# Performance work log

Measured on AMD Instinct MI355X. Metric: run time of the kernel, lower is better.

The kernel has to match this reference:

```python
import jax, jax.numpy as jnp
import numpy as np

N_NODES = 100000
N_EDGES = 1600000
IN_DIM = 128
HID_DIM = 64
OUT_DIM = 1


def setup_inputs() -> dict:
    key = jax.random.key(0)
    k = jax.random.split(key, 8)
    x = jax.random.normal(k[0], (N_NODES, IN_DIM), dtype=jnp.float32)
    edge_index = jax.random.randint(k[1], (2, N_EDGES), 0, N_NODES, dtype=jnp.int64)
    # GCNConv layer 1: weight [IN, HID], bias [HID] (glorot-ish scale)
    W1 = jax.random.normal(k[2], (IN_DIM, HID_DIM), dtype=jnp.float32) / np.sqrt(IN_DIM)
    b1 = jnp.zeros((HID_DIM,), dtype=jnp.float32)
    W2 = jax.random.normal(k[3], (HID_DIM, HID_DIM), dtype=jnp.float32) / np.sqrt(HID_DIM)
    b2 = jnp.zeros((HID_DIM,), dtype=jnp.float32)
    Wfc = jax.random.normal(k[4], (HID_DIM, OUT_DIM), dtype=jnp.float32) / np.sqrt(HID_DIM)
    bfc = jnp.zeros((OUT_DIM,), dtype=jnp.float32)
    return {"x": x, "edge_index": edge_index, "W1": W1, "b1": b1,
            "W2": W2, "b2": b2, "Wfc": Wfc, "bfc": bfc}


def _gcn_norm(edge_index, n_nodes):
    # PyG GCNConv default: add self-loops, symmetric normalization.
    src, dst = edge_index[0], edge_index[1]
    loop = jnp.arange(n_nodes, dtype=src.dtype)
    src = jnp.concatenate([src, loop])
    dst = jnp.concatenate([dst, loop])
    deg = jax.ops.segment_sum(jnp.ones_like(dst, dtype=jnp.float32), dst,
                              num_segments=n_nodes)
    deg_isqrt = jax.lax.rsqrt(deg)  # deg >= 1 thanks to self-loops
    norm = deg_isqrt[src] * deg_isqrt[dst]  # [E+N]
    return src, dst, norm


def _gcn_conv(x, src, dst, norm, W, b, n_nodes):
    h = x @ W                      # [N, D_out] dense transform first (D_out <= D_in)
    msg = h[src] * norm[:, None]   # gather + normalize  [E+N, D_out]
    out = jax.ops.segment_sum(msg, dst, num_segments=n_nodes)  # scatter-add
    return out + b


def reference(x, edge_index, W1, b1, W2, b2, Wfc, bfc):
    n = x.shape[0]
    src, dst, norm = _gcn_norm(edge_index, n)
    h = jax.nn.relu(_gcn_conv(x, src, dst, norm, W1, b1, n))
    h = jax.nn.relu(_gcn_conv(h, src, dst, norm, W2, b2, n))
    return h @ Wfc + bfc  # [N, 1]
```

## Files before the change

### kernel.cpp

```cpp
#include <hip/hip_runtime.h>
#include <hip/hip_bf16.h>


#define IN_DIM 128
#define HID 64
#define B1 256
#define MAXNC 128

typedef unsigned int uint;

__device__ inline uint pack_bf16x2(float a, float b) {
    uint ua = __builtin_bit_cast(uint, a);
    uint ub = __builtin_bit_cast(uint, b);
    ua += 0x7fffu + ((ua >> 16) & 1u);
    ub += 0x7fffu + ((ub >> 16) & 1u);
    return (ua >> 16) | (ub & 0xffff0000u);
}
__device__ inline float bf_lo(uint g) { return __builtin_bit_cast(float, g << 16); }
__device__ inline float bf_hi(uint g) { return __builtin_bit_cast(float, g & 0xffff0000u); }

__global__ __launch_bounds__(512) void hist1(const int* __restrict__ dst,
                                             int* __restrict__ ghist,
                                             int E, int NC, int chunk) {
    __shared__ int h[MAXNC];
    int t = threadIdx.x, blk = blockIdx.x;
    if (t < NC) h[t] = 0;
    __syncthreads();
    int s = blk * chunk, e = min(E, s + chunk);
    for (int i = s + t; i < e; i += 512) atomicAdd(&h[dst[i] >> 10], 1);
    __syncthreads();
    if (t < NC) ghist[(size_t)t * B1 + blk] = h[t];
}

__global__ __launch_bounds__(1024) void scan_mat(int* __restrict__ a, int M,
                                                 int* __restrict__ row_off, int N) {
    __shared__ int ws[16], wsoff[16], total_s;
    int t = threadIdx.x;
    int seg = (M + 1023) >> 10;
    int s = t * seg, e = min(M, s + seg);
    int sum = 0;
    for (int i = s; i < e; ++i) sum += a[i];
    int incl = sum;
#pragma unroll
    for (int o = 1; o < 64; o <<= 1) {
        int u = __shfl_up(incl, o, 64);
        if ((t & 63) >= o) incl += u;
    }
    if ((t & 63) == 63) ws[t >> 6] = incl;
    __syncthreads();
    if (t == 0) {
        int run = 0;
#pragma unroll
        for (int i = 0; i < 16; ++i) { wsoff[i] = run; run += ws[i]; }
        total_s = run;
    }
    __syncthreads();
    int run = wsoff[t >> 6] + incl - sum;
    for (int i = s; i < e; ++i) { int tmp = a[i]; a[i] = run; run += tmp; }
    if (t == 0) row_off[N] = total_s;
}

__global__ __launch_bounds__(512) void scatter1(const int* __restrict__ src,
                                                const int* __restrict__ dst,
                                                const int* __restrict__ goff,
                                                int2* __restrict__ pairs,
                                                int E, int NC, int chunk) {
    __shared__ int cur[MAXNC];
    int t = threadIdx.x, blk = blockIdx.x;
    if (t < NC) cur[t] = goff[(size_t)t * B1 + blk];
    __syncthreads();
    int s = blk * chunk, e = min(E, s + chunk);
    for (int i = s + t; i < e; i += 512) {
        int d = dst[i];
        int p = atomicAdd(&cur[d >> 10], 1);
        pairs[p] = make_int2(src[i], d);
    }
}

__global__ __launch_bounds__(1024) void build_csr(const int2* __restrict__ pairs,
                                                  const int* __restrict__ goff,
                                                  int* __restrict__ row_off,
                                                  float* __restrict__ disqrt,
                                                  int* __restrict__ col,
                                                  int E, int NC, int N) {
    __shared__ int h[1024], cur[1024];
    __shared__ int ws[16], wsoff[16];
    int b = blockIdx.x, t = threadIdx.x;
    int base = goff[(size_t)b * B1];
    int next = (b + 1 < NC) ? goff[(size_t)(b + 1) * B1] : E;
    h[t] = 0;
    __syncthreads();
    for (int i = base + t; i < next; i += 1024)
        atomicAdd(&h[pairs[i].y & 1023], 1);
    __syncthreads();
    int deg = h[t];
    int incl = deg;
#pragma unroll
    for (int o = 1; o < 64; o <<= 1) {
        int u = __shfl_up(incl, o, 64);
        if ((t & 63) >= o) incl += u;
    }
    if ((t & 63) == 63) ws[t >> 6] = incl;
    __syncthreads();
    if (t == 0) {
        int run = 0;
#pragma unroll
        for (int i = 0; i < 16; ++i) { wsoff[i] = run; run += ws[i]; }
    }
    __syncthreads();
    int excl = wsoff[t >> 6] + incl - deg;
    cur[t] = base + excl;
    int node = (b << 10) + t;
    if (node < N) {
        row_off[node] = base + excl;
        disqrt[node]  = rsqrtf((float)(deg + 1));
    }
    __syncthreads();
    for (int i = base + t; i < next; i += 1024) {
        int2 p = pairs[i];
        int pos = atomicAdd(&cur[p.y & 1023], 1);
        col[pos] = p.x;
    }
}

template <int K>
__global__ __launch_bounds__(256) void gemm_tile(const float* __restrict__ X,
                                                 const float* __restrict__ W,
                                                 const float* __restrict__ disqrt,
                                                 uint* __restrict__ Tsb, int n) {
    __shared__ float xs[32][68];
    __shared__ float ws[32][64];
    const int tid  = threadIdx.x;
    const int nIdx = tid & 15;
    const int mIdx = tid >> 4;
    const int m0   = blockIdx.x * 64;
    float acc[4][4] = {};
    for (int kc = 0; kc < K; kc += 32) {
        int f = tid;
#pragma unroll
        for (int i = 0; i < 2; ++i, f += 256) {
            int r  = f >> 3;
            int kq = f & 7;
            int row = m0 + r;
            float4 g = make_float4(0.f, 0.f, 0.f, 0.f);
            if (row < n) g = *(const float4*)(X + (size_t)row * K + kc + 4 * kq);
            xs[4 * kq + 0][r] = g.x;
            xs[4 * kq + 1][r] = g.y;
            xs[4 * kq + 2][r] = g.z;
            xs[4 * kq + 3][r] = g.w;
        }
        f = tid;
#pragma unroll
        for (int i = 0; i < 2; ++i, f += 256) {
            int kk = f >> 4;
            int cq = f & 15;
            *(float4*)&ws[kk][4 * cq] =
                *(const float4*)(W + (size_t)(kc + kk) * 64 + 4 * cq);
        }
        __syncthreads();
#pragma unroll 4
        for (int k = 0; k < 32; ++k) {
            float4 a = *(const float4*)&xs[k][4 * mIdx];
            float4 b = *(const float4*)&ws[k][4 * nIdx];
            const float* ap = (const float*)&a;
            const float* bp = (const float*)&b;
#pragma unroll
            for (int mi = 0; mi < 4; ++mi)
#pragma unroll
                for (int ni = 0; ni < 4; ++ni)
                    acc[mi][ni] += ap[mi] * bp[ni];
        }
        __syncthreads();
    }
#pragma unroll
    for (int mi = 0; mi < 4; ++mi) {
        int row = m0 + 4 * mIdx + mi;
        if (row < n) {
            float s = disqrt[row];
            uint2 pk;
            pk.x = pack_bf16x2(acc[mi][0] * s, acc[mi][1] * s);
            pk.y = pack_bf16x2(acc[mi][2] * s, acc[mi][3] * s);
            *(uint2*)(Tsb + (size_t)row * 32 + 2 * nIdx) = pk;
        }
    }
}

template <bool FUSE_FC>
__global__ __launch_bounds__(256) void agg_kernel(const uint* __restrict__ Tsb,
                                                  const int* __restrict__ row_off,
                                                  const int* __restrict__ col,
                                                  const float* __restrict__ disqrt,
                                                  const float* __restrict__ bias,
                                                  const float* __restrict__ wfc,
                                                  const float* __restrict__ bfc,
                                                  float* __restrict__ out, int n) {
    int node = blockIdx.x * 4 + (threadIdx.x >> 6);
    if (node >= n) return;
    int lane = threadIdx.x & 63;
    int h = lane >> 5;
    int p = lane & 31;
    float2 acc = make_float2(0.f, 0.f);
    {
        uint g = Tsb[(size_t)node * 32 + p];
        if (h == 0) { acc.x += bf_lo(g); acc.y += bf_hi(g); }
    }
    int beg = __builtin_amdgcn_readfirstlane(row_off[node]);
    int end = __builtin_amdgcn_readfirstlane(row_off[node + 1]);
    int i = beg;
    for (; i + 8 <= end; i += 8) {
        int e = i + h;
        int s0 = col[e + 0];
        int s1 = col[e + 2];
        int s2 = col[e + 4];
        int s3 = col[e + 6];
        uint g0 = Tsb[(size_t)s0 * 32 + p];
        uint g1 = Tsb[(size_t)s1 * 32 + p];
        uint g2 = Tsb[(size_t)s2 * 32 + p];
        uint g3 = Tsb[(size_t)s3 * 32 + p];
        acc.x += bf_lo(g0); acc.y += bf_hi(g0);
        acc.x += bf_lo(g1); acc.y += bf_hi(g1);
        acc.x += bf_lo(g2); acc.y += bf_hi(g2);
        acc.x += bf_lo(g3); acc.y += bf_hi(g3);
    }
    for (; i + 2 <= end; i += 2) {
        int s = col[i + h];
        uint g = Tsb[(size_t)s * 32 + p];
        acc.x += bf_lo(g); acc.y += bf_hi(g);
    }
    if (i < end) {
        int s = col[i];
        uint g = Tsb[(size_t)s * 32 + p];
        if (h == 0) { acc.x += bf_lo(g); acc.y += bf_hi(g); }
    }
    acc.x += __shfl_xor(acc.x, 32, 64);
    acc.y += __shfl_xor(acc.y, 32, 64);
    float dq = disqrt[node];
    float2 bv = *(const float2*)(bias + 2 * p);
    float rx = fmaxf(acc.x * dq + bv.x, 0.f);
    float ry = fmaxf(acc.y * dq + bv.y, 0.f);
    if (!FUSE_FC) {
        if (h == 0)
            *(float2*)(out + (size_t)node * HID + 2 * p) = make_float2(rx, ry);
    } else {
        float2 wv = *(const float2*)(wfc + 2 * p);
        float v = rx * wv.x + ry * wv.y;
        v += __shfl_down(v, 16, 64);
        v += __shfl_down(v, 8, 64);
        v += __shfl_down(v, 4, 64);
        v += __shfl_down(v, 2, 64);
        v += __shfl_down(v, 1, 64);
        if (lane == 0) out[node] = v + bfc[0];
    }
}

extern "C" void kernel_launch(void* const* d_in, const int* in_sizes, int n_in,
                              void* d_out, int out_size, void* d_ws, size_t ws_size,
                              hipStream_t stream) {
    const float* x   = (const float*)d_in[0];
    const int*   ei  = (const int*)d_in[1];
    const float* W1  = (const float*)d_in[2];
    const float* b1  = (const float*)d_in[3];
    const float* W2  = (const float*)d_in[4];
    const float* b2  = (const float*)d_in[5];
    const float* Wfc = (const float*)d_in[6];
    const float* bfc = (const float*)d_in[7];
    float* out = (float*)d_out;

    const int N = in_sizes[0] / IN_DIM;
    const int E = in_sizes[1] / 2;
    const int* src = ei;
    const int* dst = ei + E;
    const int NC    = (N + 1023) >> 10;
    const int chunk = (E + B1 - 1) / B1;

    char* w = (char*)d_ws;
    auto alloc = [&](size_t bytes) {
        void* p = (void*)w;
        w += (bytes + 255) & ~(size_t)255;
        return p;
    };
    int*   row_off = (int*)alloc((size_t)(N + 1) * 4);
    float* disqrt  = (float*)alloc((size_t)N * 4);
    int*   goff    = (int*)alloc((size_t)NC * B1 * 4);
    int*   col     = (int*)alloc((size_t)E * 4);
    size_t scrA = (size_t)E * 8, scrB = (size_t)N * HID * 2;
    void*  scr  = alloc(scrA > scrB ? scrA : scrB);
    float* h1   = (float*)alloc((size_t)N * HID * 4);
    int2*  pairs = (int2*)scr;
    uint*  Tsb   = (uint*)scr;

    hist1<<<B1, 512, 0, stream>>>(dst, goff, E, NC, chunk);
    scan_mat<<<1, 1024, 0, stream>>>(goff, NC * B1, row_off, N);
    scatter1<<<B1, 512, 0, stream>>>(src, dst, goff, pairs, E, NC, chunk);
    build_csr<<<NC, 1024, 0, stream>>>(pairs, goff, row_off, disqrt, col, E, NC, N);

    gemm_tile<IN_DIM><<<(N + 63) / 64, 256, 0, stream>>>(x, W1, disqrt, Tsb, N);
    agg_kernel<false><<<(N + 3) / 4, 256, 0, stream>>>(Tsb, row_off, col, disqrt,
                                                       b1, nullptr, nullptr, h1, N);

    gemm_tile<HID><<<(N + 63) / 64, 256, 0, stream>>>(h1, W2, disqrt, Tsb, N);
    agg_kernel<true><<<(N + 3) / 4, 256, 0, stream>>>(Tsb, row_off, col, disqrt,
                                                      b2, Wfc, bfc, out, N);
}
```

Measured before the change: 320.1 us.

## Prefetch GEMM tiles into registers and batch column-index loads via wave shuffles

The GEMM kernel now loads the next K-chunk of X and W into registers while the current shared-memory tile is being consumed, which overlaps global loads with FMAs. The inner loop unroll also rises to 8. The aggregation kernel loads up to 64 column indices per wave with one coalesced load and hands them out with shuffles, and it unrolls to 8 outstanding gathers per half-wave, which cuts dependent index-load latency. The cost is higher register pressure and extra shuffle instructions.

```diff
diff --git a/kernel.cpp b/kernel.cpp
--- a/kernel.cpp
+++ b/kernel.cpp
@@ -134,31 +134,34 @@
     const int nIdx = tid & 15;
     const int mIdx = tid >> 4;
     const int m0   = blockIdx.x * 64;
+    const int r0 = tid >> 3, kq = tid & 7, r1 = r0 + 32;
+    const int wk = tid >> 4, wc = tid & 15;
+    const int row0 = m0 + r0, row1 = m0 + r1;
+    const float4 z4 = make_float4(0.f, 0.f, 0.f, 0.f);
+
+    float4 gx0 = (row0 < n) ? *(const float4*)(X + (size_t)row0 * K + 4 * kq) : z4;
+    float4 gx1 = (row1 < n) ? *(const float4*)(X + (size_t)row1 * K + 4 * kq) : z4;
+    float4 gw0 = *(const float4*)(W + (size_t)wk * 64 + 4 * wc);
+    float4 gw1 = *(const float4*)(W + (size_t)(wk + 16) * 64 + 4 * wc);
+
     float acc[4][4] = {};
-    for (int kc = 0; kc < K; kc += 32) {
-        int f = tid;
-#pragma unroll
-        for (int i = 0; i < 2; ++i, f += 256) {
-            int r  = f >> 3;
-            int kq = f & 7;
-            int row = m0 + r;
-            float4 g = make_float4(0.f, 0.f, 0.f, 0.f);
-            if (row < n) g = *(const float4*)(X + (size_t)row * K + kc + 4 * kq);
-            xs[4 * kq + 0][r] = g.x;
-            xs[4 * kq + 1][r] = g.y;
-            xs[4 * kq + 2][r] = g.z;
-            xs[4 * kq + 3][r] = g.w;
-        }
-        f = tid;
-#pragma unroll
-        for (int i = 0; i < 2; ++i, f += 256) {
-            int kk = f >> 4;
-            int cq = f & 15;
-            *(float4*)&ws[kk][4 * cq] =
-                *(const float4*)(W + (size_t)(kc + kk) * 64 + 4 * cq);
-        }
+    for (int kc = 0;;) {
+        xs[4 * kq + 0][r0] = gx0.x; xs[4 * kq + 1][r0] = gx0.y;
+        xs[4 * kq + 2][r0] = gx0.z; xs[4 * kq + 3][r0] = gx0.w;
+        xs[4 * kq + 0][r1] = gx1.x; xs[4 * kq + 1][r1] = gx1.y;
+        xs[4 * kq + 2][r1] = gx1.z; xs[4 * kq + 3][r1] = gx1.w;
+        *(float4*)&ws[wk][4 * wc]      = gw0;
+        *(float4*)&ws[wk + 16][4 * wc] = gw1;
         __syncthreads();
-#pragma unroll 4
+        kc += 32;
+        const bool more = kc < K;
+        if (more) {
+            gx0 = (row0 < n) ? *(const float4*)(X + (size_t)row0 * K + kc + 4 * kq) : z4;
+            gx1 = (row1 < n) ? *(const float4*)(X + (size_t)row1 * K + kc + 4 * kq) : z4;
+            gw0 = *(const float4*)(W + (size_t)(kc + wk) * 64 + 4 * wc);
+            gw1 = *(const float4*)(W + (size_t)(kc + wk + 16) * 64 + 4 * wc);
+        }
+#pragma unroll 8
         for (int k = 0; k < 32; ++k) {
             float4 a = *(const float4*)&xs[k][4 * mIdx];
             float4 b = *(const float4*)&ws[k][4 * nIdx];
@@ -170,6 +173,7 @@
                 for (int ni = 0; ni < 4; ++ni)
                     acc[mi][ni] += ap[mi] * bp[ni];
         }
+        if (!more) break;
         __syncthreads();
     }
 #pragma unroll
@@ -202,35 +206,51 @@
     float2 acc = make_float2(0.f, 0.f);
     {
         uint g = Tsb[(size_t)node * 32 + p];
-        if (h == 0) { acc.x += bf_lo(g); acc.y += bf_hi(g); }
+        if (h == 0) { acc.x = bf_lo(g); acc.y = bf_hi(g); }
     }
     int beg = __builtin_amdgcn_readfirstlane(row_off[node]);
     int end = __builtin_amdgcn_readfirstlane(row_off[node + 1]);
-    int i = beg;
-    for (; i + 8 <= end; i += 8) {
-        int e = i + h;
-        int s0 = col[e + 0];
-        int s1 = col[e + 2];
-        int s2 = col[e + 4];
-        int s3 = col[e + 6];
-        uint g0 = Tsb[(size_t)s0 * 32 + p];
-        uint g1 = Tsb[(size_t)s1 * 32 + p];
-        uint g2 = Tsb[(size_t)s2 * 32 + p];
-        uint g3 = Tsb[(size_t)s3 * 32 + p];
-        acc.x += bf_lo(g0); acc.y += bf_hi(g0);
-        acc.x += bf_lo(g1); acc.y += bf_hi(g1);
-        acc.x += bf_lo(g2); acc.y += bf_hi(g2);
-        acc.x += bf_lo(g3); acc.y += bf_hi(g3);
-    }
-    for (; i + 2 <= end; i += 2) {
-        int s = col[i + h];
-        uint g = Tsb[(size_t)s * 32 + p];
-        acc.x += bf_lo(g); acc.y += bf_hi(g);
-    }
-    if (i < end) {
-        int s = col[i];
-        uint g = Tsb[(size_t)s * 32 + p];
-        if (h == 0) { acc.x += bf_lo(g); acc.y += bf_hi(g); }
+    for (int batch = beg; batch < end; batch += 64) {
+        int bn = min(64, end - batch);
+        int cv = 0;
+        if (batch + lane < end) cv = col[batch + lane];
+        int j = 0;
+        for (; j + 16 <= bn; j += 16) {
+            int s0 = __shfl(cv, j + 0 + h, 64);
+            int s1 = __shfl(cv, j + 2 + h, 64);
+            int s2 = __shfl(cv, j + 4 + h, 64);
+            int s3 = __shfl(cv, j + 6 + h, 64);
+            int s4 = __shfl(cv, j + 8 + h, 64);
+            int s5 = __shfl(cv, j + 10 + h, 64);
+            int s6 = __shfl(cv, j + 12 + h, 64);
+            int s7 = __shfl(cv, j + 14 + h, 64);
+            uint g0 = Tsb[(size_t)s0 * 32 + p];
+            uint g1 = Tsb[(size_t)s1 * 32 + p];
+            uint g2 = Tsb[(size_t)s2 * 32 + p];
+            uint g3 = Tsb[(size_t)s3 * 32 + p];
+            uint g4 = Tsb[(size_t)s4 * 32 + p];
+            uint g5 = Tsb[(size_t)s5 * 32 + p];
+            uint g6 = Tsb[(size_t)s6 * 32 + p];
+            uint g7 = Tsb[(size_t)s7 * 32 + p];
+            acc.x += bf_lo(g0); acc.y += bf_hi(g0);
+            acc.x += bf_lo(g1); acc.y += bf_hi(g1);
+            acc.x += bf_lo(g2); acc.y += bf_hi(g2);
+            acc.x += bf_lo(g3); acc.y += bf_hi(g3);
+            acc.x += bf_lo(g4); acc.y += bf_hi(g4);
+            acc.x += bf_lo(g5); acc.y += bf_hi(g5);
+            acc.x += bf_lo(g6); acc.y += bf_hi(g6);
+            acc.x += bf_lo(g7); acc.y += bf_hi(g7);
+        }
+        for (; j + 2 <= bn; j += 2) {
+            int s = __shfl(cv, j + h, 64);
+            uint g = Tsb[(size_t)s * 32 + p];
+            acc.x += bf_lo(g); acc.y += bf_hi(g);
+        }
+        if (j < bn) {
+            int s = __shfl(cv, j, 64);
+            uint g = Tsb[(size_t)s * 32 + p];
+            if (h == 0) { acc.x += bf_lo(g); acc.y += bf_hi(g); }
+        }
     }
     acc.x += __shfl_xor(acc.x, 32, 64);
     acc.y += __shfl_xor(acc.y, 32, 64);
```

Measured after the change: 320.9 us. No clear change (+0.3%).
